# Kernel optimization log

Measured on AMD Instinct MI355X. Metric: run time of the kernel, lower is better.

Reference implementation:

```python
import jax, jax.numpy as jnp
import numpy as np

B, H, S, D = 2, 12, 4096, 64

def setup_inputs() -> dict:
    key = jax.random.key(0)
    kq, kk, kv = jax.random.split(key, 3)
    Q = jax.random.normal(kq, (B, H, S, D), dtype=jnp.float32)
    K = jax.random.normal(kk, (B, H, S, D), dtype=jnp.float32)
    V = jax.random.normal(kv, (B, H, S, D), dtype=jnp.float32)
    attn_mask = jnp.zeros((1, 1, 1, 1), dtype=bool)  # unused by the original forward
    return {"Q": Q, "K": K, "V": V, "attn_mask": attn_mask}

def reference(Q, K, V, attn_mask):
    d_k = K.shape[3]
    # scores: [B, H, S, S] -- naive full materialization, matching the original
    scores = jnp.einsum("bhqd,bhkd->bhqk", Q, K) / np.sqrt(d_k).astype(Q.dtype)
    attn = jax.nn.softmax(scores, axis=-1)
    context = jnp.einsum("bhqk,bhkd->bhqd", attn, V)
    return context
```

## Files before the change

kernel.cpp:

```cpp
#include <hip/hip_runtime.h>

typedef _Float16 half4_t __attribute__((ext_vector_type(4)));
typedef _Float16 half8_t __attribute__((ext_vector_type(8)));
typedef float floatx4 __attribute__((ext_vector_type(4)));

constexpr int S_  = 4096;
constexpr int D_  = 64;
constexpr int NBH = 24;
constexpr int BM  = 128;
constexpr int BN  = 64;
constexpr float SC2 = 0.125f * 1.44269504088896340736f;


__global__ __launch_bounds__(256) void convert_f32_f16(
    const float* __restrict__ src, _Float16* __restrict__ dst, float scale)
{
  int i = (blockIdx.x * 256 + threadIdx.x) * 8;
  float4 a = *(const float4*)(src + i);
  float4 b = *(const float4*)(src + i + 4);
  half8_t h = { (_Float16)(a.x*scale),(_Float16)(a.y*scale),(_Float16)(a.z*scale),(_Float16)(a.w*scale),
                (_Float16)(b.x*scale),(_Float16)(b.y*scale),(_Float16)(b.z*scale),(_Float16)(b.w*scale) };
  *(half8_t*)(dst + i) = h;
}

__global__ __launch_bounds__(256) void transpose_v(
    const float* __restrict__ V, _Float16* __restrict__ Vh)
{
  __shared__ float tile[64 * 68];
  const int kt = blockIdx.x, bh = blockIdx.y, tid = threadIdx.x;
  const size_t vbase = (size_t)bh * S_ * D_;
#pragma unroll
  for (int it = 0; it < 4; ++it) {
    int r  = (tid >> 4) + 16 * it;
    int c4 = (tid & 15) * 4;
    float4 v = *(const float4*)(V + vbase + (size_t)(kt * 64 + r) * D_ + c4);
    *(float4*)(&tile[r * 68 + c4]) = v;
  }
  __syncthreads();
  const int d = tid >> 2, cb = (tid & 3) * 16;
  _Float16 out[16];
#pragma unroll
  for (int j = 0; j < 16; ++j) {
    int key = 16 * (j >> 2) + 4 * (tid & 3) + (j & 3);
    out[j] = (_Float16)tile[key * 68 + d];
  }
  _Float16* dst = Vh + (((size_t)(bh * 64 + kt) * 64 + d) << 6) + cb;
  *(half8_t*)(dst)     = *(half8_t*)(&out[0]);
  *(half8_t*)(dst + 8) = *(half8_t*)(&out[8]);
}


__device__ __forceinline__ void async16(const _Float16* g, _Float16* l) {
  __builtin_amdgcn_global_load_lds((const __attribute__((address_space(1))) void*)g,
                                   (__attribute__((address_space(3))) void*)l, 16, 0, 0);
}


__global__ __launch_bounds__(256, 3) void fattn_f16(
    const _Float16* __restrict__ Qh, const _Float16* __restrict__ Kh,
    const _Float16* __restrict__ Vh, float* __restrict__ O)
{
  __shared__ __align__(16) _Float16 Ks[2][4096];
  __shared__ __align__(16) _Float16 Vs[2][4096];

  const int tid  = threadIdx.x;
  const int lane = tid & 63;
  const int w    = tid >> 6;
  const int g    = lane >> 4;
  const int m    = lane & 15;

  const int bid  = blockIdx.x;
  const int xcd  = bid & 7;
  const int slot = bid >> 3;
  const int bh   = xcd * 3 + (slot >> 5);
  const int qblk = slot & 31;
  const size_t base = (size_t)bh * S_ * D_;
  const int q0 = qblk * BM + w * 32;

  half8_t qf[2][2];
#pragma unroll
  for (int qt = 0; qt < 2; ++qt)
#pragma unroll
    for (int ks = 0; ks < 2; ++ks)
      qf[qt][ks] = *(const half8_t*)(Qh + base + (size_t)(q0 + qt*16 + m) * D_ + 8*g + 32*ks);

  floatx4 oacc[2][4];
#pragma unroll
  for (int qt = 0; qt < 2; ++qt)
#pragma unroll
    for (int db = 0; db < 4; ++db) oacc[qt][db] = (floatx4){0.f,0.f,0.f,0.f};
  float lsum[2] = {0.f, 0.f};

  const int srow0 = tid >> 3;
  const int scol  = ((tid & 7) ^ ((tid >> 3) & 7)) * 8;
  const int goff0 = srow0 * 64 + scol;
  const int goff1 = (srow0 + 32) * 64 + scol;
  const int lbase0 = (w * 64) * 8;
  const int lbase1 = (w * 64 + 256) * 8;

  const _Float16* Kbh = Kh + base;
  const _Float16* Vbh = Vh + ((size_t)bh << 18);

  auto stage = [&](int buf, int kt) {
    const _Float16* Kt = Kbh + ((size_t)kt << 12);
    const _Float16* Vt = Vbh + ((size_t)kt << 12);
    async16(Kt + goff0, &Ks[buf][lbase0]);
    async16(Kt + goff1, &Ks[buf][lbase1]);
    async16(Vt + goff0, &Vs[buf][lbase0]);
    async16(Vt + goff1, &Vs[buf][lbase1]);
  };

  stage(0, 0);
  __syncthreads();

  int buf = 0;
  for (int kt = 0; kt < S_ / BN; ++kt) {
    if (kt + 1 < S_ / BN) stage(buf ^ 1, kt + 1);

    const _Float16* Kd = Ks[buf];
    const _Float16* Vd = Vs[buf];
    const int r7 = m & 7;

    half8_t kf[4][2];
#pragma unroll
    for (int nb = 0; nb < 4; ++nb) {
      kf[nb][0] = *(const half8_t*)(&Kd[(16*nb + m) * 64 + ((g    ) ^ r7) * 8]);
      kf[nb][1] = *(const half8_t*)(&Kd[(16*nb + m) * 64 + ((g + 4) ^ r7) * 8]);
    }
    half4_t vf[4][4];
#pragma unroll
    for (int db = 0; db < 4; ++db)
#pragma unroll
      for (int p = 0; p < 2; ++p) {
        half8_t v8 = *(const half8_t*)(&Vd[(16*db + m) * 64 + ((2*g + p) ^ r7) * 8]);
        vf[2*p  ][db] = (half4_t){v8[0], v8[1], v8[2], v8[3]};
        vf[2*p+1][db] = (half4_t){v8[4], v8[5], v8[6], v8[7]};
      }

#pragma unroll
    for (int qt = 0; qt < 2; ++qt) {
      floatx4 sacc[4];
#pragma unroll
      for (int nb = 0; nb < 4; ++nb) {
        floatx4 acc = (floatx4){0.f,0.f,0.f,0.f};
        acc = __builtin_amdgcn_mfma_f32_16x16x32_f16(kf[nb][0], qf[qt][0], acc, 0, 0, 0);
        acc = __builtin_amdgcn_mfma_f32_16x16x32_f16(kf[nb][1], qf[qt][1], acc, 0, 0, 0);
        sacc[nb] = acc;
      }
      half4_t pf[4];
      float ls = 0.f;
#pragma unroll
      for (int nb = 0; nb < 4; ++nb) {
        float p0 = __builtin_amdgcn_exp2f(sacc[nb][0]);
        float p1 = __builtin_amdgcn_exp2f(sacc[nb][1]);
        float p2 = __builtin_amdgcn_exp2f(sacc[nb][2]);
        float p3 = __builtin_amdgcn_exp2f(sacc[nb][3]);
        ls += p0 + p1 + p2 + p3;
        pf[nb] = (half4_t){ (_Float16)p0, (_Float16)p1, (_Float16)p2, (_Float16)p3 };
      }
      lsum[qt] += ls;
#pragma unroll
      for (int nb = 0; nb < 4; ++nb)
#pragma unroll
        for (int db = 0; db < 4; ++db)
          oacc[qt][db] = __builtin_amdgcn_mfma_f32_16x16x16f16(pf[nb], vf[nb][db], oacc[qt][db], 0, 0, 0);
    }

    __syncthreads();
    buf ^= 1;
  }

#pragma unroll
  for (int qt = 0; qt < 2; ++qt) {
    float l = lsum[qt];
    l += __shfl_xor(l, 16);
    l += __shfl_xor(l, 32);
    floatx4 linv;
#pragma unroll
    for (int r = 0; r < 4; ++r)
      linv[r] = 1.0f / __shfl(l, (lane & 48) + 4*g + r);
    float* Op = O + base + (size_t)(q0 + qt*16) * D_;
#pragma unroll
    for (int db = 0; db < 4; ++db)
#pragma unroll
      for (int r = 0; r < 4; ++r)
        Op[(size_t)(4*g + r) * D_ + 16*db + m] = oacc[qt][db][r] * linv[r];
  }
}


constexpr int SKf = 72;
constexpr int SVf = 68;

__global__ __launch_bounds__(256, 3) void fattn_fb(
    const float* __restrict__ Q, const float* __restrict__ K,
    const float* __restrict__ V, float* __restrict__ O)
{
  __shared__ __align__(16) _Float16 Ks[2][64 * SKf];
  __shared__ __align__(16) _Float16 Vs[2][64 * SVf];
  const int tid = threadIdx.x, lane = tid & 63, w = tid >> 6, g = lane >> 4, m = lane & 15;
  const int bid = blockIdx.x, xcd = bid & 7, slot = bid >> 3;
  const int bh = xcd * 3 + (slot >> 5), qblk = slot & 31;
  const size_t base = (size_t)bh * S_ * D_;
  const int q0 = qblk * BM + w * 32;
  half8_t qf[2][2];
#pragma unroll
  for (int qt = 0; qt < 2; ++qt)
#pragma unroll
    for (int ks = 0; ks < 2; ++ks) {
      const float4* qp = (const float4*)(Q + base + (size_t)(q0 + qt*16 + m) * D_ + 8*g + 32*ks);
      float4 a = qp[0], b = qp[1];
      qf[qt][ks] = (half8_t){ (_Float16)(a.x*SC2),(_Float16)(a.y*SC2),(_Float16)(a.z*SC2),(_Float16)(a.w*SC2),
                              (_Float16)(b.x*SC2),(_Float16)(b.y*SC2),(_Float16)(b.z*SC2),(_Float16)(b.w*SC2) };
    }
  floatx4 oacc[2][4];
#pragma unroll
  for (int qt = 0; qt < 2; ++qt)
#pragma unroll
    for (int db = 0; db < 4; ++db) oacc[qt][db] = (floatx4){0.f,0.f,0.f,0.f};
  float lsum[2] = {0.f, 0.f};
  const float* Kb = K + base; const float* Vb = V + base;
  float4 kreg[4]; float vreg[16];
  const int sL = ((lane >> 2) ^ (lane >> 4)) & 3;
  auto issue = [&](int kt) {
    const float* Kt = Kb + (size_t)kt * BN * D_;
#pragma unroll
    for (int it = 0; it < 2; ++it) {
      int sl = tid + 256*it; int key = sl >> 3; int c8 = (sl & 7) << 3;
      const float4* p = (const float4*)(Kt + (size_t)key * D_ + c8);
      kreg[2*it] = p[0]; kreg[2*it+1] = p[1];
    }
    const float* Vt = Vb + (size_t)kt * BN * D_;
#pragma unroll
    for (int it = 0; it < 4; ++it) {
      int kb = it * 16 + (w << 2);
      const float* vp = Vt + (size_t)kb * D_ + lane;
      vreg[4*it+0]=vp[0]; vreg[4*it+1]=vp[D_]; vreg[4*it+2]=vp[2*D_]; vreg[4*it+3]=vp[3*D_];
    }
  };
  auto commit = [&](int buf) {
    _Float16* Kd = Ks[buf]; _Float16* Vd = Vs[buf];
#pragma unroll
    for (int it = 0; it < 2; ++it) {
      int sl = tid + 256*it; int key = sl >> 3; int c8 = (sl & 7) << 3;
      float4 a = kreg[2*it], b = kreg[2*it+1];
      *(half8_t*)(&Kd[key * SKf + c8]) = (half8_t){ (_Float16)a.x,(_Float16)a.y,(_Float16)a.z,(_Float16)a.w,
                                                    (_Float16)b.x,(_Float16)b.y,(_Float16)b.z,(_Float16)b.w };
    }
#pragma unroll
    for (int it = 0; it < 4; ++it)
      *(half4_t*)(&Vd[lane * SVf + 4 * ((4*it + w) ^ sL)]) =
        (half4_t){ (_Float16)vreg[4*it+0], (_Float16)vreg[4*it+1], (_Float16)vreg[4*it+2], (_Float16)vreg[4*it+3] };
  };
  issue(0); commit(0); __syncthreads();
  const int s0 = m >> 2;
  for (int kt = 0; kt < S_ / BN; ++kt) {
    const int cur = kt & 1;
    if (kt < 63) issue(kt + 1);
    const _Float16* Kd = Ks[cur]; const _Float16* Vd = Vs[cur];
    half8_t kf[4][2];
#pragma unroll
    for (int nb = 0; nb < 4; ++nb) {
      kf[nb][0] = *(const half8_t*)(&Kd[(16*nb + m) * SKf + 8*g]);
      kf[nb][1] = *(const half8_t*)(&Kd[(16*nb + m) * SKf + 8*g + 32]);
    }
    half4_t vf[4][4];
#pragma unroll
    for (int nb = 0; nb < 4; ++nb)
#pragma unroll
      for (int db = 0; db < 4; ++db)
        vf[nb][db] = *(const half4_t*)(&Vd[(16*db + m) * SVf + 4 * ((4*nb + g) ^ s0 ^ db)]);
#pragma unroll
    for (int qt = 0; qt < 2; ++qt) {
      floatx4 sacc[4];
#pragma unroll
      for (int nb = 0; nb < 4; ++nb) {
        floatx4 acc = (floatx4){0.f,0.f,0.f,0.f};
        acc = __builtin_amdgcn_mfma_f32_16x16x32_f16(kf[nb][0], qf[qt][0], acc, 0, 0, 0);
        acc = __builtin_amdgcn_mfma_f32_16x16x32_f16(kf[nb][1], qf[qt][1], acc, 0, 0, 0);
        sacc[nb] = acc;
      }
      half4_t pf[4]; float ls = 0.f;
#pragma unroll
      for (int nb = 0; nb < 4; ++nb) {
        float p0 = __builtin_amdgcn_exp2f(sacc[nb][0]); float p1 = __builtin_amdgcn_exp2f(sacc[nb][1]);
        float p2 = __builtin_amdgcn_exp2f(sacc[nb][2]); float p3 = __builtin_amdgcn_exp2f(sacc[nb][3]);
        ls += p0 + p1 + p2 + p3;
        pf[nb] = (half4_t){ (_Float16)p0, (_Float16)p1, (_Float16)p2, (_Float16)p3 };
      }
      lsum[qt] += ls;
#pragma unroll
      for (int nb = 0; nb < 4; ++nb)
#pragma unroll
        for (int db = 0; db < 4; ++db)
          oacc[qt][db] = __builtin_amdgcn_mfma_f32_16x16x16f16(pf[nb], vf[nb][db], oacc[qt][db], 0, 0, 0);
    }
    if (kt < 63) commit(1 - cur);
    __syncthreads();
  }
#pragma unroll
  for (int qt = 0; qt < 2; ++qt) {
    float l = lsum[qt];
    l += __shfl_xor(l, 16); l += __shfl_xor(l, 32);
    floatx4 linv;
#pragma unroll
    for (int r = 0; r < 4; ++r) linv[r] = 1.0f / __shfl(l, (lane & 48) + 4*g + r);
    float* Op = O + base + (size_t)(q0 + qt*16) * D_;
#pragma unroll
    for (int db = 0; db < 4; ++db)
#pragma unroll
      for (int r = 0; r < 4; ++r)
        Op[(size_t)(4*g + r) * D_ + 16*db + m] = oacc[qt][db][r] * linv[r];
  }
}

extern "C" void kernel_launch(void* const* d_in, const int* in_sizes, int n_in,
                              void* d_out, int out_size, void* d_ws, size_t ws_size,
                              hipStream_t stream) {
  const float* Q = (const float*)d_in[0];
  const float* K = (const float*)d_in[1];
  const float* V = (const float*)d_in[2];
  float* Out = (float*)d_out;

  constexpr size_t NELEM = (size_t)NBH * S_ * D_;
  constexpr size_t NEED  = 3 * NELEM * sizeof(_Float16);

  if (ws_size >= NEED) {
    _Float16* Qh = (_Float16*)d_ws;
    _Float16* Kh = Qh + NELEM;
    _Float16* Vh = Kh + NELEM;
    convert_f32_f16<<<NELEM / 2048, 256, 0, stream>>>(Q, Qh, SC2);
    convert_f32_f16<<<NELEM / 2048, 256, 0, stream>>>(K, Kh, 1.0f);
    transpose_v<<<dim3(64, NBH), 256, 0, stream>>>(V, Vh);
    fattn_f16<<<NBH * (S_ / BM), 256, 0, stream>>>(Qh, Kh, Vh, Out);
  } else {
    fattn_fb<<<NBH * (S_ / BM), 256, 0, stream>>>(Q, K, V, Out);
  }
}
```

Measured before the change: 235.5 us.

## Split key tile across warps, triple-buffer K/V, fuse K/V preconversion

Merges the K conversion and V transpose into one preprocessing kernel and drops the separate Q conversion: Q is read as fp32 and cast inside the attention kernel, with the softmax scale folded into K. The attention kernel now has each warp handle 64 queries and half of every 64-key tile, and the two halves' partial outputs and row sums are combined through shared memory at the end. K/V staging moves from double to triple buffering, with a manual waitcnt and barrier so loads run two tiles ahead. This cuts launches and preprocessing traffic and gives more reuse per K/V fragment read, at the cost of more registers per thread and a final cross-warp reduction.

After: 218.8 us. -7.1%, faster.

```diff
diff --git a/kernel.cpp b/kernel.cpp
--- a/kernel.cpp
+++ b/kernel.cpp
@@ -11,40 +11,37 @@
 constexpr int BN  = 64;
 constexpr float SC2 = 0.125f * 1.44269504088896340736f;
 
-
-__global__ __launch_bounds__(256) void convert_f32_f16(
-    const float* __restrict__ src, _Float16* __restrict__ dst, float scale)
-{
-  int i = (blockIdx.x * 256 + threadIdx.x) * 8;
-  float4 a = *(const float4*)(src + i);
-  float4 b = *(const float4*)(src + i + 4);
-  half8_t h = { (_Float16)(a.x*scale),(_Float16)(a.y*scale),(_Float16)(a.z*scale),(_Float16)(a.w*scale),
-                (_Float16)(b.x*scale),(_Float16)(b.y*scale),(_Float16)(b.z*scale),(_Float16)(b.w*scale) };
-  *(half8_t*)(dst + i) = h;
-}
-
-__global__ __launch_bounds__(256) void transpose_v(
-    const float* __restrict__ V, _Float16* __restrict__ Vh)
+__global__ __launch_bounds__(256) void preconv(
+    const float* __restrict__ K, const float* __restrict__ V,
+    _Float16* __restrict__ Kh, _Float16* __restrict__ Vh)
 {
   __shared__ float tile[64 * 68];
   const int kt = blockIdx.x, bh = blockIdx.y, tid = threadIdx.x;
-  const size_t vbase = (size_t)bh * S_ * D_;
+  const size_t tbase = ((size_t)bh * 64 + kt) * 4096;
+#pragma unroll
+  for (int it = 0; it < 2; ++it) {
+    size_t i = tbase + (size_t)(tid + 256 * it) * 8;
+    float4 a = *(const float4*)(K + i);
+    float4 b = *(const float4*)(K + i + 4);
+    *(half8_t*)(Kh + i) = (half8_t){
+      (_Float16)(a.x*SC2),(_Float16)(a.y*SC2),(_Float16)(a.z*SC2),(_Float16)(a.w*SC2),
+      (_Float16)(b.x*SC2),(_Float16)(b.y*SC2),(_Float16)(b.z*SC2),(_Float16)(b.w*SC2) };
+  }
 #pragma unroll
   for (int it = 0; it < 4; ++it) {
     int r  = (tid >> 4) + 16 * it;
     int c4 = (tid & 15) * 4;
-    float4 v = *(const float4*)(V + vbase + (size_t)(kt * 64 + r) * D_ + c4);
-    *(float4*)(&tile[r * 68 + c4]) = v;
+    *(float4*)(&tile[r * 68 + c4]) = *(const float4*)(V + tbase + (size_t)r * 64 + c4);
   }
   __syncthreads();
-  const int d = tid >> 2, cb = (tid & 3) * 16;
+  const int d = tid >> 2;
   _Float16 out[16];
 #pragma unroll
   for (int j = 0; j < 16; ++j) {
     int key = 16 * (j >> 2) + 4 * (tid & 3) + (j & 3);
     out[j] = (_Float16)tile[key * 68 + d];
   }
-  _Float16* dst = Vh + (((size_t)(bh * 64 + kt) * 64 + d) << 6) + cb;
+  _Float16* dst = Vh + tbase + (size_t)d * 64 + (tid & 3) * 16;
   *(half8_t*)(dst)     = *(half8_t*)(&out[0]);
   *(half8_t*)(dst + 8) = *(half8_t*)(&out[8]);
 }
@@ -55,19 +52,19 @@
                                    (__attribute__((address_space(3))) void*)l, 16, 0, 0);
 }
 
-
-__global__ __launch_bounds__(256, 3) void fattn_f16(
-    const _Float16* __restrict__ Qh, const _Float16* __restrict__ Kh,
+__global__ __launch_bounds__(256, 3) void fattn2(
+    const float* __restrict__ Qf, const _Float16* __restrict__ Kh,
     const _Float16* __restrict__ Vh, float* __restrict__ O)
 {
-  __shared__ __align__(16) _Float16 Ks[2][4096];
-  __shared__ __align__(16) _Float16 Vs[2][4096];
+  __shared__ __align__(16) _Float16 smem[6 * 4096];
 
   const int tid  = threadIdx.x;
   const int lane = tid & 63;
   const int w    = tid >> 6;
   const int g    = lane >> 4;
   const int m    = lane & 15;
+  const int qh   = w & 1;
+  const int kh2  = w >> 1;
 
   const int bid  = blockIdx.x;
   const int xcd  = bid & 7;
@@ -75,123 +72,147 @@
   const int bh   = xcd * 3 + (slot >> 5);
   const int qblk = slot & 31;
   const size_t base = (size_t)bh * S_ * D_;
-  const int q0 = qblk * BM + w * 32;
-
-  half8_t qf[2][2];
-#pragma unroll
-  for (int qt = 0; qt < 2; ++qt)
-#pragma unroll
-    for (int ks = 0; ks < 2; ++ks)
-      qf[qt][ks] = *(const half8_t*)(Qh + base + (size_t)(q0 + qt*16 + m) * D_ + 8*g + 32*ks);
-
-  floatx4 oacc[2][4];
-#pragma unroll
-  for (int qt = 0; qt < 2; ++qt)
+  const int q0g = qblk * BM + qh * 64;
+
+  half8_t qf[4][2];
+#pragma unroll
+  for (int qt = 0; qt < 4; ++qt)
+#pragma unroll
+    for (int ks = 0; ks < 2; ++ks) {
+      const float4* qp = (const float4*)(Qf + base + (size_t)(q0g + qt*16 + m) * D_ + 8*g + 32*ks);
+      float4 a = qp[0], b = qp[1];
+      qf[qt][ks] = (half8_t){ (_Float16)a.x,(_Float16)a.y,(_Float16)a.z,(_Float16)a.w,
+                              (_Float16)b.x,(_Float16)b.y,(_Float16)b.z,(_Float16)b.w };
+    }
+
+  floatx4 oacc[4][4];
+#pragma unroll
+  for (int qt = 0; qt < 4; ++qt)
 #pragma unroll
     for (int db = 0; db < 4; ++db) oacc[qt][db] = (floatx4){0.f,0.f,0.f,0.f};
-  float lsum[2] = {0.f, 0.f};
-
-  const int srow0 = tid >> 3;
-  const int scol  = ((tid & 7) ^ ((tid >> 3) & 7)) * 8;
-  const int goff0 = srow0 * 64 + scol;
-  const int goff1 = (srow0 + 32) * 64 + scol;
-  const int lbase0 = (w * 64) * 8;
-  const int lbase1 = (w * 64 + 256) * 8;
-
-  const _Float16* Kbh = Kh + base;
-  const _Float16* Vbh = Vh + ((size_t)bh << 18);
-
-  auto stage = [&](int buf, int kt) {
-    const _Float16* Kt = Kbh + ((size_t)kt << 12);
-    const _Float16* Vt = Vbh + ((size_t)kt << 12);
-    async16(Kt + goff0, &Ks[buf][lbase0]);
-    async16(Kt + goff1, &Ks[buf][lbase1]);
-    async16(Vt + goff0, &Vs[buf][lbase0]);
-    async16(Vt + goff1, &Vs[buf][lbase1]);
+  float lsum[4] = {0.f, 0.f, 0.f, 0.f};
+
+  const int goff0 = (tid >> 3) * 64 + (((tid & 7) ^ ((tid >> 3) & 7)) << 3);
+  const int goff1 = goff0 + 2048;
+  const int l0 = w * 512;
+  const int l1 = l0 + 2048;
+
+  const _Float16* Kb = Kh + base;
+  const _Float16* Vb = Vh + base;
+
+  _Float16 *k0 = smem,          *k1 = smem + 4096,  *k2 = smem + 8192;
+  _Float16 *v0 = smem + 12288,  *v1 = smem + 16384, *v2 = smem + 20480;
+
+  auto stage = [&](_Float16* kd, _Float16* vd, int kt) {
+    const _Float16* Kt = Kb + ((size_t)kt << 12);
+    const _Float16* Vt = Vb + ((size_t)kt << 12);
+    async16(Kt + goff0, kd + l0);
+    async16(Kt + goff1, kd + l1);
+    async16(Vt + goff0, vd + l0);
+    async16(Vt + goff1, vd + l1);
   };
 
-  stage(0, 0);
+  stage(k0, v0, 0);
+  stage(k1, v1, 1);
+
+  const int r7 = m & 7;
+  const int krow = 32 * kh2 + m;
+
+  for (int kt = 0; kt < 64; ++kt) {
+    asm volatile("s_waitcnt vmcnt(4)\n\ts_barrier" ::: "memory");
+    stage(k2, v2, (kt + 2) & 63);
+
+    half8_t kf[2][2];
+#pragma unroll
+    for (int nb2 = 0; nb2 < 2; ++nb2) {
+      kf[nb2][0] = *(const half8_t*)(&k0[(krow + 16*nb2) * 64 + ((g    ) ^ r7) * 8]);
+      kf[nb2][1] = *(const half8_t*)(&k0[(krow + 16*nb2) * 64 + ((g + 4) ^ r7) * 8]);
+    }
+    half4_t vf[2][4];
+#pragma unroll
+    for (int db = 0; db < 4; ++db) {
+      half8_t v8 = *(const half8_t*)(&v0[(16*db + m) * 64 + ((2*g + kh2) ^ r7) * 8]);
+      vf[0][db] = (half4_t){v8[0], v8[1], v8[2], v8[3]};
+      vf[1][db] = (half4_t){v8[4], v8[5], v8[6], v8[7]};
+    }
+
+#pragma unroll
+    for (int qt = 0; qt < 4; ++qt) {
+      floatx4 s0 = (floatx4){0.f,0.f,0.f,0.f};
+      floatx4 s1 = (floatx4){0.f,0.f,0.f,0.f};
+      s0 = __builtin_amdgcn_mfma_f32_16x16x32_f16(kf[0][0], qf[qt][0], s0, 0, 0, 0);
+      s0 = __builtin_amdgcn_mfma_f32_16x16x32_f16(kf[0][1], qf[qt][1], s0, 0, 0, 0);
+      s1 = __builtin_amdgcn_mfma_f32_16x16x32_f16(kf[1][0], qf[qt][0], s1, 0, 0, 0);
+      s1 = __builtin_amdgcn_mfma_f32_16x16x32_f16(kf[1][1], qf[qt][1], s1, 0, 0, 0);
+
+      float p0 = __builtin_amdgcn_exp2f(s0[0]);
+      float p1 = __builtin_amdgcn_exp2f(s0[1]);
+      float p2 = __builtin_amdgcn_exp2f(s0[2]);
+      float p3 = __builtin_amdgcn_exp2f(s0[3]);
+      float p4 = __builtin_amdgcn_exp2f(s1[0]);
+      float p5 = __builtin_amdgcn_exp2f(s1[1]);
+      float p6 = __builtin_amdgcn_exp2f(s1[2]);
+      float p7 = __builtin_amdgcn_exp2f(s1[3]);
+      lsum[qt] += (p0 + p1 + p2 + p3) + (p4 + p5 + p6 + p7);
+      half4_t pf0 = (half4_t){ (_Float16)p0, (_Float16)p1, (_Float16)p2, (_Float16)p3 };
+      half4_t pf1 = (half4_t){ (_Float16)p4, (_Float16)p5, (_Float16)p6, (_Float16)p7 };
+
+#pragma unroll
+      for (int db = 0; db < 4; ++db) {
+        oacc[qt][db] = __builtin_amdgcn_mfma_f32_16x16x16f16(pf0, vf[0][db], oacc[qt][db], 0, 0, 0);
+        oacc[qt][db] = __builtin_amdgcn_mfma_f32_16x16x16f16(pf1, vf[1][db], oacc[qt][db], 0, 0, 0);
+      }
+    }
+
+    _Float16* t;
+    t = k0; k0 = k1; k1 = k2; k2 = t;
+    t = v0; v0 = v1; v1 = v2; v2 = t;
+  }
+
   __syncthreads();
-
-  int buf = 0;
-  for (int kt = 0; kt < S_ / BN; ++kt) {
-    if (kt + 1 < S_ / BN) stage(buf ^ 1, kt + 1);
-
-    const _Float16* Kd = Ks[buf];
-    const _Float16* Vd = Vs[buf];
-    const int r7 = m & 7;
-
-    half8_t kf[4][2];
-#pragma unroll
-    for (int nb = 0; nb < 4; ++nb) {
-      kf[nb][0] = *(const half8_t*)(&Kd[(16*nb + m) * 64 + ((g    ) ^ r7) * 8]);
-      kf[nb][1] = *(const half8_t*)(&Kd[(16*nb + m) * 64 + ((g + 4) ^ r7) * 8]);
-    }
-    half4_t vf[4][4];
-#pragma unroll
-    for (int db = 0; db < 4; ++db)
-#pragma unroll
-      for (int p = 0; p < 2; ++p) {
-        half8_t v8 = *(const half8_t*)(&Vd[(16*db + m) * 64 + ((2*g + p) ^ r7) * 8]);
-        vf[2*p  ][db] = (half4_t){v8[0], v8[1], v8[2], v8[3]};
-        vf[2*p+1][db] = (half4_t){v8[4], v8[5], v8[6], v8[7]};
+  float* red  = (float*)smem;
+  float* lred = red + 8704;
+  const int ro = qh * 4352;
+
+  if (kh2 == 1) {
+#pragma unroll
+    for (int qt = 0; qt < 4; ++qt) {
+#pragma unroll
+      for (int db = 0; db < 4; ++db)
+        *(floatx4*)(&red[ro + (16*db + m) * 68 + qt*16 + 4*g]) = oacc[qt][db];
+      float l = lsum[qt];
+      l += __shfl_xor(l, 16);
+      l += __shfl_xor(l, 32);
+      lred[qh * 64 + qt*16 + m] = l;
+    }
+  }
+  __syncthreads();
+  if (kh2 == 0) {
+#pragma unroll
+    for (int qt = 0; qt < 4; ++qt) {
+      float l = lsum[qt];
+      l += __shfl_xor(l, 16);
+      l += __shfl_xor(l, 32);
+      l += lred[qh * 64 + qt*16 + m];
+      floatx4 linv;
+#pragma unroll
+      for (int r = 0; r < 4; ++r)
+        linv[r] = 1.0f / __shfl(l, (lane & 48) + 4*g + r);
+      float* Op = O + base + (size_t)(q0g + qt*16) * D_;
+#pragma unroll
+      for (int db = 0; db < 4; ++db) {
+        floatx4 part = *(const floatx4*)(&red[ro + (16*db + m) * 68 + qt*16 + 4*g]);
+        floatx4 o = oacc[qt][db] + part;
+#pragma unroll
+        for (int r = 0; r < 4; ++r)
+          Op[(size_t)(4*g + r) * D_ + 16*db + m] = o[r] * linv[r];
       }
-
-#pragma unroll
-    for (int qt = 0; qt < 2; ++qt) {
-      floatx4 sacc[4];
-#pragma unroll
-      for (int nb = 0; nb < 4; ++nb) {
-        floatx4 acc = (floatx4){0.f,0.f,0.f,0.f};
-        acc = __builtin_amdgcn_mfma_f32_16x16x32_f16(kf[nb][0], qf[qt][0], acc, 0, 0, 0);
-        acc = __builtin_amdgcn_mfma_f32_16x16x32_f16(kf[nb][1], qf[qt][1], acc, 0, 0, 0);
-        sacc[nb] = acc;
-      }
-      half4_t pf[4];
-      float ls = 0.f;
-#pragma unroll
-      for (int nb = 0; nb < 4; ++nb) {
-        float p0 = __builtin_amdgcn_exp2f(sacc[nb][0]);
-        float p1 = __builtin_amdgcn_exp2f(sacc[nb][1]);
-        float p2 = __builtin_amdgcn_exp2f(sacc[nb][2]);
-        float p3 = __builtin_amdgcn_exp2f(sacc[nb][3]);
-        ls += p0 + p1 + p2 + p3;
-        pf[nb] = (half4_t){ (_Float16)p0, (_Float16)p1, (_Float16)p2, (_Float16)p3 };
-      }
-      lsum[qt] += ls;
-#pragma unroll
-      for (int nb = 0; nb < 4; ++nb)
-#pragma unroll
-        for (int db = 0; db < 4; ++db)
-          oacc[qt][db] = __builtin_amdgcn_mfma_f32_16x16x16f16(pf[nb], vf[nb][db], oacc[qt][db], 0, 0, 0);
-    }
-
-    __syncthreads();
-    buf ^= 1;
-  }
-
-#pragma unroll
-  for (int qt = 0; qt < 2; ++qt) {
-    float l = lsum[qt];
-    l += __shfl_xor(l, 16);
-    l += __shfl_xor(l, 32);
-    floatx4 linv;
-#pragma unroll
-    for (int r = 0; r < 4; ++r)
-      linv[r] = 1.0f / __shfl(l, (lane & 48) + 4*g + r);
-    float* Op = O + base + (size_t)(q0 + qt*16) * D_;
-#pragma unroll
-    for (int db = 0; db < 4; ++db)
-#pragma unroll
-      for (int r = 0; r < 4; ++r)
-        Op[(size_t)(4*g + r) * D_ + 16*db + m] = oacc[qt][db][r] * linv[r];
-  }
-}
-
+    }
+  }
+}
 
 constexpr int SKf = 72;
 constexpr int SVf = 68;
-
 __global__ __launch_bounds__(256, 3) void fattn_fb(
     const float* __restrict__ Q, const float* __restrict__ K,
     const float* __restrict__ V, float* __restrict__ O)
@@ -253,8 +274,8 @@
         (half4_t){ (_Float16)vreg[4*it+0], (_Float16)vreg[4*it+1], (_Float16)vreg[4*it+2], (_Float16)vreg[4*it+3] };
   };
   issue(0); commit(0); __syncthreads();
-  const int s0 = m >> 2;
-  for (int kt = 0; kt < S_ / BN; ++kt) {
+  const int s0i = m >> 2;
+  for (int kt = 0; kt < 64; ++kt) {
     const int cur = kt & 1;
     if (kt < 63) issue(kt + 1);
     const _Float16* Kd = Ks[cur]; const _Float16* Vd = Vs[cur];
@@ -269,7 +290,7 @@
     for (int nb = 0; nb < 4; ++nb)
 #pragma unroll
       for (int db = 0; db < 4; ++db)
-        vf[nb][db] = *(const half4_t*)(&Vd[(16*db + m) * SVf + 4 * ((4*nb + g) ^ s0 ^ db)]);
+        vf[nb][db] = *(const half4_t*)(&Vd[(16*db + m) * SVf + 4 * ((4*nb + g) ^ s0i ^ db)]);
 #pragma unroll
     for (int qt = 0; qt < 2; ++qt) {
       floatx4 sacc[4];
@@ -323,16 +344,13 @@
   float* Out = (float*)d_out;
 
   constexpr size_t NELEM = (size_t)NBH * S_ * D_;
-  constexpr size_t NEED  = 3 * NELEM * sizeof(_Float16);
+  constexpr size_t NEED  = 2 * NELEM * sizeof(_Float16);
 
   if (ws_size >= NEED) {
-    _Float16* Qh = (_Float16*)d_ws;
-    _Float16* Kh = Qh + NELEM;
-    _Float16* Vh = Kh + NELEM;
-    convert_f32_f16<<<NELEM / 2048, 256, 0, stream>>>(Q, Qh, SC2);
-    convert_f32_f16<<<NELEM / 2048, 256, 0, stream>>>(K, Kh, 1.0f);
-    transpose_v<<<dim3(64, NBH), 256, 0, stream>>>(V, Vh);
-    fattn_f16<<<NBH * (S_ / BM), 256, 0, stream>>>(Qh, Kh, Vh, Out);
+    _Float16* Khp = (_Float16*)d_ws;
+    _Float16* Vhp = Khp + NELEM;
+    preconv<<<dim3(64, NBH), 256, 0, stream>>>(K, V, Khp, Vhp);
+    fattn2<<<NBH * (S_ / BM), 256, 0, stream>>>(Q, Khp, Vhp, Out);
   } else {
     fattn_fb<<<NBH * (S_ / BM), 256, 0, stream>>>(Q, K, V, Out);
   }
```
